# Kernel optimization log

Measured on AMD Instinct MI355X. Metric: run time of the kernel, lower is better.

## Reference

```python
import jax, jax.numpy as jnp
import numpy as np

# cfg constants (init_kwargs)
NMS_THRESH = 0.6
CONF_THRESH = 0.05
TOPN = 1000           # nms_thresh_topN: pre-NMS cap and post-NMS cap
NUM_CLASSES = 80
CLS_OFFSET = 4096.0   # > max image coord; class-aware NMS via coordinate offset


def setup_inputs() -> dict:
    key = jax.random.key(0)
    k0, k1, k2, k3 = jax.random.split(key, 4)
    B, H, W, C = 16, 128, 128, NUM_CLASSES
    N = H * W
    image_h, image_w = 1024, 1024
    # anchor-point pixel coordinates for this FPN level
    locations = jax.random.uniform(k0, (N, 2), dtype=jnp.float32) * 1024.0
    pred_cls = jax.random.normal(k1, (B, H, W, C), dtype=jnp.float32)
    # (l, t, r, b) distances are positive
    pred_boxes = jax.random.uniform(k2, (B, H, W, 4), dtype=jnp.float32) * 64.0
    pred_centerness = jax.random.normal(k3, (B, H, W), dtype=jnp.float32)
    return {"locations": locations, "pred_cls": pred_cls, "pred_boxes": pred_boxes,
            "pred_centerness": pred_centerness, "image_h": image_h, "image_w": image_w}


def _pairwise_iou(b):  # b: [K, 4] xyxy
    x1, y1, x2, y2 = b[:, 0], b[:, 1], b[:, 2], b[:, 3]
    area = jnp.maximum(x2 - x1, 0.0) * jnp.maximum(y2 - y1, 0.0)
    ix1 = jnp.maximum(x1[:, None], x1[None, :])
    iy1 = jnp.maximum(y1[:, None], y1[None, :])
    ix2 = jnp.minimum(x2[:, None], x2[None, :])
    iy2 = jnp.minimum(y2[:, None], y2[None, :])
    inter = jnp.maximum(ix2 - ix1, 0.0) * jnp.maximum(iy2 - iy1, 0.0)
    return inter / (area[:, None] + area[None, :] - inter + 1e-9)


def _nms_keep(iou, valid):
    # greedy NMS over score-descending candidates; iou: [B,K,K], valid: [B,K] bool
    K = iou.shape[-1]
    ar = jnp.arange(K)

    def body(i, keep):
        iou_i = jax.lax.dynamic_index_in_dim(iou, i, axis=1, keepdims=False)  # [B,K]
        keep_i = jnp.take(keep, i, axis=1)                                    # [B]
        sup = (iou_i > NMS_THRESH) & (ar[None, :] > i) & keep_i[:, None]
        return keep & ~sup

    return jax.lax.fori_loop(0, K, body, valid)


def reference(locations, pred_cls, pred_boxes, pred_centerness, image_h, image_w):
    B, H, W, C = pred_cls.shape
    N = H * W
    cls = jax.nn.sigmoid(pred_cls.reshape(B, N, C))
    ctr = jax.nn.sigmoid(pred_centerness.reshape(B, N))
    boxes = pred_boxes.reshape(B, N, 4)
    scores = cls * ctr[:, :, None]                    # [B,N,C]
    mask = cls > CONF_THRESH
    neg = jnp.asarray(-jnp.inf, scores.dtype)
    flat = jnp.where(mask, scores, neg).reshape(B, N * C)
    # pre-NMS top-K over masked (location, class) candidates; emulates
    # cls_mask_top_n = clamp(mask.sum(), max=topN) + topk in the torch code
    vals, idx = jax.lax.top_k(flat, TOPN)             # [B,K]
    valid = jnp.isfinite(vals)
    loc_i = idx // C                                  # location index
    lab = idx % C + 1                                 # 1-based class label
    pb = jnp.take_along_axis(boxes, loc_i[:, :, None], axis=1)   # [B,K,4] (l,t,r,b)
    locs = locations[loc_i]                                       # [B,K,2]
    x1 = jnp.clip(locs[..., 0] - pb[..., 0], 0.0, image_w - 1)
    y1 = jnp.clip(locs[..., 1] - pb[..., 1], 0.0, image_h - 1)
    x2 = jnp.clip(locs[..., 0] + pb[..., 2], 0.0, image_w - 1)
    y2 = jnp.clip(locs[..., 1] + pb[..., 3], 0.0, image_h - 1)
    det = jnp.stack([x1, y1, x2, y2], axis=-1)        # [B,K,4] xyxy, clipped
    score = jnp.where(valid, vals, 0.0)
    # sort by score descending for greedy NMS
    order = jnp.argsort(-score, axis=1)
    score = jnp.take_along_axis(score, order, axis=1)
    valid = jnp.take_along_axis(valid, order, axis=1)
    lab = jnp.take_along_axis(lab, order, axis=1)
    det = jnp.take_along_axis(det, order[:, :, None], axis=1)
    # per-class NMS via class-offset trick (boxes of different classes never overlap)
    iou = jax.vmap(_pairwise_iou)(det + lab.astype(det.dtype)[:, :, None] * CLS_OFFSET)
    keep = _nms_keep(iou, valid) & valid
    # final topN (nms_thresh_topN) is a no-op here: candidates <= TOPN already
    boxes_out = det * keep[:, :, None].astype(det.dtype)
    scores_out = jnp.where(keep, score, 0.0)
    labels_out = jnp.where(keep, lab, 0)
    return boxes_out, scores_out, labels_out
```

## Files before the change

kernel.cpp:

```cpp
#include <hip/hip_runtime.h>

#define B_    16
#define N_    16384
#define C_    80
#define NC_   (N_ * C_)
#define TOPN_ 1000
#define SEGCAP_ 4096
#define T0_   0.70f
#define T0KEY_ 0x3F333333u
#define RKEY_  0x3E800000u
#define NBIN_  4096

#define OFF_CNT    0u
#define ZERO_BYTES 8192u
#define OFF_CAND   8192u
#define OFF_DET    4202496u
#define OFF_DETO   4464640u
#define OFF_SCORE  4726784u
#define OFF_LAB    4792320u
#define OFF_VALID  4857856u
#define OFF_COL    4859904u

__device__ __forceinline__ float sigm(float x) { return 1.0f / (1.0f + expf(-x)); }

__device__ __forceinline__ int binof(unsigned key) {
    int b = (int)((key - RKEY_) >> 12);
    return b > (NBIN_ - 1) ? (NBIN_ - 1) : b;
}
__device__ __forceinline__ unsigned key_lb(int b) {
    return RKEY_ + ((unsigned)b << 12);
}

__global__ __launch_bounds__(256, 4) void k_pass1(const float* __restrict__ cls,
                                                  const float* __restrict__ ctr,
                                                  unsigned* __restrict__ cntp,
                                                  unsigned long long* __restrict__ cand) {
    __shared__ float xh[64];
    __shared__ float sbv[64];
    __shared__ unsigned long long stage[512];
    __shared__ unsigned lcnt, gbase, lcw;
    const int blk = blockIdx.x, t = threadIdx.x;
    const int b = blk >> 8, k = blk & 255;
    const int shard = k & 7;
    if (t == 0) lcnt = 0;
    if (t < 64) {
        float sc = sigm(ctr[b * N_ + k * 64 + t]);
        sbv[t] = sc;
        float q = T0_ / sc;
        xh[t] = (q < 1.f) ? (logf(q / (1.f - q)) - 1e-3f) : 3.0e38f;
    }
    __syncthreads();
    const float4* p = (const float4*)(cls + (size_t)b * NC_ + (size_t)k * 5120);
    float4 v[5];
    #pragma unroll
    for (int i = 0; i < 5; ++i) v[i] = p[5 * t + i];
    const int r = t >> 2;
    const float thr = xh[r];
    float mx = v[0].x;
    #pragma unroll
    for (int i = 0; i < 5; ++i)
        mx = fmaxf(mx, fmaxf(fmaxf(v[i].x, v[i].y), fmaxf(v[i].z, v[i].w)));
    if (mx >= thr) {
        const float sb = sbv[r];
        #pragma unroll
        for (int i = 0; i < 5; ++i) {
            float xs[4] = {v[i].x, v[i].y, v[i].z, v[i].w};
            #pragma unroll
            for (int j = 0; j < 4; ++j) {
                if (xs[j] >= thr) {
                    float sapx = sb * __builtin_amdgcn_rcpf(1.f + __expf(-xs[j]));
                    if (sapx >= T0_ * 0.999f) {
                        float s = sigm(xs[j]);
                        unsigned key = __float_as_uint(s * sb);
                        if (key >= T0KEY_) {
                            unsigned pos = atomicAdd(&lcnt, 1u);
                            if (pos < 512u) {
                                unsigned e = (unsigned)(k * 5120 + (5 * t + i) * 4 + j);
                                stage[pos] = ((unsigned long long)key << 32) |
                                             (unsigned long long)(0xFFFFFFFFu - e);
                            }
                        }
                    }
                }
            }
        }
    }
    __syncthreads();
    if (t == 0) {
        unsigned lc = lcnt; if (lc > 512u) lc = 512u;
        gbase = atomicAdd(&cntp[b * 128 + shard * 16], lc);
        lcw = lc;
    }
    __syncthreads();
    unsigned long long* seg = cand + ((size_t)(b * 8 + shard) << 12);
    for (unsigned i = t; i < lcw; i += 256) {
        unsigned gp = gbase + i;
        if (gp < SEGCAP_) seg[gp] = stage[i];
    }
}

__global__ __launch_bounds__(256) void k_rescue(const float* __restrict__ cls,
                                                const float* __restrict__ ctr,
                                                unsigned* __restrict__ cntp,
                                                unsigned long long* __restrict__ cand) {
    const int blk = blockIdx.x, t = threadIdx.x;
    const int b = blk >> 7, k = blk & 127;
    {
        unsigned tot = 0;
        #pragma unroll
        for (int s = 0; s < 8; ++s) tot += cntp[b * 128 + s * 16];
        if (tot >= (unsigned)TOPN_) return;
    }
    const int shard = k & 7;
    __shared__ float xh[128];
    __shared__ float sbv[128];
    __shared__ unsigned long long stage[1024];
    __shared__ unsigned lcnt, gbase, lcw;
    if (t == 0) lcnt = 0;
    if (t < 128) {
        float sc = sigm(ctr[b * N_ + k * 128 + t]);
        sbv[t] = sc;
        float q = 0.25f / sc;
        xh[t] = (q < 1.f) ? (logf(q / (1.f - q)) - 1e-3f) : 3.0e38f;
    }
    __syncthreads();
    const float4* p = (const float4*)(cls + (size_t)b * NC_ + (size_t)k * 10240);
    for (int f = t; f < 2560; f += 256) {
        float4 v = p[f];
        int nl = f / 20;
        float thr = xh[nl];
        float mx = fmaxf(fmaxf(v.x, v.y), fmaxf(v.z, v.w));
        if (mx >= thr) {
            float sb = sbv[nl];
            float xs[4] = {v.x, v.y, v.z, v.w};
            #pragma unroll
            for (int j = 0; j < 4; ++j) {
                if (xs[j] >= thr) {
                    float s = sigm(xs[j]);
                    if (s > 0.05f) {
                        unsigned key = __float_as_uint(s * sb);
                        if (key >= RKEY_ && key < T0KEY_) {
                            unsigned pos = atomicAdd(&lcnt, 1u);
                            if (pos < 1024u) {
                                unsigned e = (unsigned)(k * 2560 + f) * 4u + (unsigned)j;
                                stage[pos] = ((unsigned long long)key << 32) |
                                             (unsigned long long)(0xFFFFFFFFu - e);
                            }
                        }
                    }
                }
            }
        }
    }
    __syncthreads();
    if (t == 0) {
        unsigned lc = lcnt; if (lc > 1024u) lc = 1024u;
        gbase = atomicAdd(&cntp[b * 128 + shard * 16], lc);
        lcw = lc;
    }
    __syncthreads();
    unsigned long long* seg = cand + ((size_t)(b * 8 + shard) << 12);
    for (unsigned i = t; i < lcw; i += 256) {
        unsigned gp = gbase + i;
        if (gp < SEGCAP_) seg[gp] = stage[i];
    }
}

__global__ __launch_bounds__(1024) void k_select(
        const unsigned long long* __restrict__ cand, const unsigned* __restrict__ cntp,
        const float* __restrict__ boxes, const float* __restrict__ locs,
        const int* __restrict__ ph, const int* __restrict__ pw,
        float4* __restrict__ det, float4* __restrict__ deto,
        float* __restrict__ score, int* __restrict__ lab,
        unsigned long long* __restrict__ validmask) {
    __shared__ unsigned hbin[NBIN_];
    __shared__ unsigned binBase[NBIN_];
    __shared__ unsigned long long srt[2048];
    __shared__ unsigned long long srt2[1024];
    __shared__ unsigned csh[8];
    __shared__ unsigned Lsh;
    const int b = blockIdx.x, t = threadIdx.x;
    if (t < 8) { unsigned cc = cntp[b * 128 + t * 16]; csh[t] = cc > SEGCAP_ ? SEGCAP_ : cc; }
    #pragma unroll
    for (int i = 0; i < 4; ++i) hbin[t + 1024 * i] = 0;
    srt[t] = 0ull; srt[t + 1024] = 0ull;
    srt2[t] = 0ull;
    __syncthreads();
    const unsigned long long* g = cand + ((size_t)b << 15);
    for (int s = 0; s < 8; ++s) {
        unsigned cc = csh[s];
        const unsigned long long* gs = g + ((size_t)s << 12);
        for (unsigned o = t; o < cc; o += 1024)
            atomicAdd(&hbin[binof((unsigned)(gs[o] >> 32))], 1u);
    }
    __syncthreads();
    if (t < 64) {
        const int l = t;
        unsigned cs = 0;
        for (int i = 0; i < 64; ++i) cs += hbin[64 * l + i];
        unsigned S = cs;
        #pragma unroll
        for (int off = 1; off < 64; off <<= 1) {
            unsigned y = __shfl_down(S, off, 64);
            if (l + off < 64) S += y;
        }
        unsigned acc = S - cs;
        int bc_l = NBIN_;
        for (int b2 = 63; b2 >= 0; --b2) {
            int bin = 64 * l + b2;
            binBase[bin] = acc;
            if (acc < (unsigned)TOPN_) bc_l = bin;
            acc += hbin[bin];
        }
        #pragma unroll
        for (int off = 1; off < 64; off <<= 1) {
            int y = __shfl_down(bc_l, off, 64);
            bc_l = bc_l < y ? bc_l : y;
        }
        if (l == 0) Lsh = key_lb(bc_l < NBIN_ ? bc_l : 0);
    }
    __syncthreads();
    const unsigned Lk = Lsh;
    for (int s = 0; s < 8; ++s) {
        unsigned cc = csh[s];
        const unsigned long long* gs = g + ((size_t)s << 12);
        for (unsigned o = t; o < cc; o += 1024) {
            unsigned long long comp = gs[o];
            unsigned key = (unsigned)(comp >> 32);
            if (key >= Lk) {
                unsigned slot = atomicAdd(&binBase[binof(key)], 1u);
                if (slot < 2048u) srt[slot] = comp;
            }
        }
    }
    __syncthreads();
    #pragma unroll
    for (int pp = 0; pp < 2; ++pp) {
        unsigned p = (unsigned)t + 1024u * pp;
        unsigned long long comp = srt[p];
        if (comp) {
            int bin = binof((unsigned)(comp >> 32));
            unsigned endq = binBase[bin];
            unsigned pop = hbin[bin];
            unsigned beg = endq - pop;
            unsigned end2 = endq > 2048u ? 2048u : endq;
            unsigned rank = 0;
            for (unsigned j = beg; j < end2; ++j) rank += (srt[j] > comp);
            unsigned pos = beg + rank;
            if (pos < 1024u) srt2[pos] = comp;
        }
    }
    __syncthreads();
    unsigned long long comp = srt2[t];
    unsigned key = (unsigned)(comp >> 32);
    float4 d = {0.f, 0.f, 0.f, 0.f}, doff = {0.f, 0.f, 0.f, 0.f};
    float sc = 0.f; int lb = 0;
    if (key) {
        unsigned idx = 0xFFFFFFFFu - (unsigned)comp;
        unsigned loc = idx / (unsigned)C_;
        unsigned cc = idx - loc * (unsigned)C_;
        lb = (int)cc + 1;
        float4 pb = ((const float4*)boxes)[(size_t)b * N_ + loc];
        float lx = locs[2 * loc], ly = locs[2 * loc + 1];
        float Wm1 = (float)(pw[0] - 1), Hm1 = (float)(ph[0] - 1);
        d.x = fminf(fmaxf(lx - pb.x, 0.f), Wm1);
        d.y = fminf(fmaxf(ly - pb.y, 0.f), Hm1);
        d.z = fminf(fmaxf(lx + pb.z, 0.f), Wm1);
        d.w = fminf(fmaxf(ly + pb.w, 0.f), Hm1);
        sc = __uint_as_float(key);
        float off = (float)lb * 4096.0f;
        doff.x = d.x + off; doff.y = d.y + off; doff.z = d.z + off; doff.w = d.w + off;
    }
    unsigned long long ball = __ballot(key != 0u);
    if ((t & 63) == 0) validmask[b * 16 + (t >> 6)] = ball;
    det[b * 1024 + t] = d;
    deto[b * 1024 + t] = doff;
    score[b * 1024 + t] = sc;
    lab[b * 1024 + t] = lb;
}

__global__ void k_col(const float4* __restrict__ deto, unsigned long long* __restrict__ colsup) {
    __shared__ float4 bx[1024];
    const int b = blockIdx.y;
    for (int i = threadIdx.x; i < 1024; i += blockDim.x) bx[i] = deto[b * 1024 + i];
    __syncthreads();
    int t = threadIdx.x;
    int i = blockIdx.x * 16 + (t >> 4);
    int w = t & 15;
    int j0 = w * 64;
    unsigned long long m = 0;
    if (i < TOPN_ && j0 < i) {
        float4 A = bx[i];
        float aA = fmaxf(A.z - A.x, 0.f) * fmaxf(A.w - A.y, 0.f);
        int jmax = i - j0; if (jmax > 64) jmax = 64;
        #pragma unroll 4
        for (int jj = 0; jj < jmax; ++jj) {
            float4 Bv = bx[j0 + jj];
            float aB = fmaxf(Bv.z - Bv.x, 0.f) * fmaxf(Bv.w - Bv.y, 0.f);
            float ix1 = fmaxf(A.x, Bv.x), iy1 = fmaxf(A.y, Bv.y);
            float ix2 = fminf(A.z, Bv.z), iy2 = fminf(A.w, Bv.w);
            float inter = fmaxf(ix2 - ix1, 0.f) * fmaxf(iy2 - iy1, 0.f);
            float iou = inter / (aA + aB - inter + 1e-9f);
            if (iou > 0.6f) m |= (1ull << jj);
        }
    }
    colsup[((size_t)b * 1024 + i) * 16 + w] = m;
}

__global__ __launch_bounds__(1024) void k_nmsout(
        const unsigned long long* __restrict__ colsup,
        const unsigned long long* __restrict__ validmask,
        const float4* __restrict__ det, const float* __restrict__ score,
        const int* __restrict__ lab, float* __restrict__ out) {
    __shared__ unsigned long long keepw[16];
    const int b = blockIdx.x, t = threadIdx.x;
    if (t < 64) {
        const int ii = t;
        const unsigned long long* Cb = colsup + (size_t)b * 16384;
        unsigned long long K[16];
        unsigned long long col[16], coln[16];
        #pragma unroll
        for (int w = 0; w < 16; ++w) col[w] = Cb[(size_t)ii * 16 + w];
        unsigned long long vword[16];
        #pragma unroll
        for (int g = 0; g < 16; ++g) vword[g] = validmask[b * 16 + g];
        #pragma unroll
        for (int g = 0; g < 16; ++g) {
            if (g < 15) {
                #pragma unroll
                for (int w = 0; w < 16; ++w)
                    coln[w] = Cb[(size_t)((g + 1) * 64 + ii) * 16 + w];
            }
            unsigned long long supprior = 0;
            #pragma unroll
            for (int w = 0; w < 16; ++w) if (w < g) supprior |= K[w] & col[w];
            bool alive = (((vword[g] >> ii) & 1ull) != 0) && (supprior == 0);
            unsigned long long diag = col[g];
            unsigned long long undec = __ballot(alive);
            unsigned long long kept = 0;
            while (undec) {
                bool meU = ((undec >> ii) & 1ull) != 0;
                bool supK = (kept & diag) != 0;
                bool anyU = (undec & diag) != 0;
                unsigned long long bkm = __ballot(meU && !supK && !anyU);
                unsigned long long brm = __ballot(meU && supK);
                kept |= bkm;
                undec &= ~(bkm | brm);
            }
            K[g] = kept;
            if (ii == 0) keepw[g] = kept;
            #pragma unroll
            for (int w = 0; w < 16; ++w) col[w] = coln[w];
        }
    }
    __syncthreads();
    if (t < TOPN_) {
        bool kp = ((keepw[t >> 6] >> (t & 63)) & 1ull) != 0;
        float4 d = det[b * 1024 + t];
        ((float4*)out)[(size_t)b * TOPN_ + t] = kp ? d : make_float4(0.f, 0.f, 0.f, 0.f);
        out[B_ * TOPN_ * 4 + b * TOPN_ + t] = kp ? score[b * 1024 + t] : 0.f;
        out[B_ * TOPN_ * 5 + b * TOPN_ + t] = kp ? (float)lab[b * 1024 + t] : 0.f;
    }
}

extern "C" void kernel_launch(void* const* d_in, const int* in_sizes, int n_in,
                              void* d_out, int out_size, void* d_ws, size_t ws_size,
                              hipStream_t stream) {
    (void)in_sizes; (void)n_in; (void)out_size; (void)ws_size;
    const float* locations = (const float*)d_in[0];
    const float* pred_cls  = (const float*)d_in[1];
    const float* pred_box  = (const float*)d_in[2];
    const float* pred_ctr  = (const float*)d_in[3];
    const int*   ph        = (const int*)d_in[4];
    const int*   pw        = (const int*)d_in[5];
    float* out = (float*)d_out;

    char* w = (char*)d_ws;
    unsigned* cntp               = (unsigned*)(w + OFF_CNT);
    unsigned long long* cand     = (unsigned long long*)(w + OFF_CAND);
    float4* det                  = (float4*)(w + OFF_DET);
    float4* deto                 = (float4*)(w + OFF_DETO);
    float* score                 = (float*)(w + OFF_SCORE);
    int* lab                     = (int*)(w + OFF_LAB);
    unsigned long long* validmsk = (unsigned long long*)(w + OFF_VALID);
    unsigned long long* colsup   = (unsigned long long*)(w + OFF_COL);

    hipMemsetAsync(w, 0, ZERO_BYTES, stream);

    k_pass1<<<4096, 256, 0, stream>>>(pred_cls, pred_ctr, cntp, cand);
    k_rescue<<<2048, 256, 0, stream>>>(pred_cls, pred_ctr, cntp, cand);
    k_select<<<B_, 1024, 0, stream>>>(cand, cntp, pred_box, locations, ph, pw,
                                      det, deto, score, lab, validmsk);
    k_col<<<dim3(64, B_), 256, 0, stream>>>(deto, colsup);
    k_nmsout<<<B_, 1024, 0, stream>>>(colsup, validmsk, det, score, lab, out);
}
```

Measured before the change: 196.1 us.

## Fuse rescue, select, IoU and NMS into one per-image tail kernel with class buckets

Merges the rescue pass, top-K selection, pairwise IoU mask construction and greedy NMS into a single 1024-thread block per image. The shared memory of the sort phase is reused for the NMS phase through a union. IoU is now computed only between candidates of the same class, bucketed in shared memory, and stored as short suppressor lists rather than a dense bitmask. This removes three kernel launches and the global-memory round trips for det, score, label and the column masks. In exchange, the rare rescue path becomes a serial 16-block scan, and the suppressor list is capped at 14 per box, which could change results if a box has more same-class overlaps than that.

```diff
diff --git a/kernel.cpp b/kernel.cpp
--- a/kernel.cpp
+++ b/kernel.cpp
@@ -14,12 +14,6 @@
 #define OFF_CNT    0u
 #define ZERO_BYTES 8192u
 #define OFF_CAND   8192u
-#define OFF_DET    4202496u
-#define OFF_DETO   4464640u
-#define OFF_SCORE  4726784u
-#define OFF_LAB    4792320u
-#define OFF_VALID  4857856u
-#define OFF_COL    4859904u
 
 __device__ __forceinline__ float sigm(float x) { return 1.0f / (1.0f + expf(-x)); }
 
@@ -99,105 +93,86 @@
     }
 }
 
-__global__ __launch_bounds__(256) void k_rescue(const float* __restrict__ cls,
-                                                const float* __restrict__ ctr,
-                                                unsigned* __restrict__ cntp,
-                                                unsigned long long* __restrict__ cand) {
-    const int blk = blockIdx.x, t = threadIdx.x;
-    const int b = blk >> 7, k = blk & 127;
-    {
-        unsigned tot = 0;
-        #pragma unroll
-        for (int s = 0; s < 8; ++s) tot += cntp[b * 128 + s * 16];
-        if (tot >= (unsigned)TOPN_) return;
-    }
-    const int shard = k & 7;
-    __shared__ float xh[128];
-    __shared__ float sbv[128];
-    __shared__ unsigned long long stage[1024];
-    __shared__ unsigned lcnt, gbase, lcw;
-    if (t == 0) lcnt = 0;
-    if (t < 128) {
-        float sc = sigm(ctr[b * N_ + k * 128 + t]);
-        sbv[t] = sc;
-        float q = 0.25f / sc;
-        xh[t] = (q < 1.f) ? (logf(q / (1.f - q)) - 1e-3f) : 3.0e38f;
-    }
-    __syncthreads();
-    const float4* p = (const float4*)(cls + (size_t)b * NC_ + (size_t)k * 10240);
-    for (int f = t; f < 2560; f += 256) {
-        float4 v = p[f];
-        int nl = f / 20;
-        float thr = xh[nl];
-        float mx = fmaxf(fmaxf(v.x, v.y), fmaxf(v.z, v.w));
-        if (mx >= thr) {
-            float sb = sbv[nl];
+union TailSMem {
+    struct {
+        unsigned hbin[NBIN_];
+        unsigned binBase[NBIN_];
+        unsigned long long srt[2048];
+        unsigned long long srt2[1024];
+    } s;
+    struct {
+        float4 bxo[1024];
+        unsigned short clsList[1024];
+        unsigned clsStart[81];
+        unsigned clsCur[81];
+        unsigned short supIdx[1024 * 14];
+    } c;
+};
+
+__global__ __launch_bounds__(1024) void k_tail(
+        unsigned long long* __restrict__ cand, unsigned* __restrict__ cntp,
+        const float* __restrict__ boxes, const float* __restrict__ locs,
+        const int* __restrict__ ph, const int* __restrict__ pw,
+        const float* __restrict__ cls, const float* __restrict__ ctr,
+        float* __restrict__ out) {
+    __shared__ TailSMem u;
+    __shared__ unsigned csh[8];
+    __shared__ unsigned Lsh;
+    __shared__ unsigned long long keepw[16];
+    const int b = blockIdx.x, t = threadIdx.x;
+
+    if (t < 8) { unsigned cc = cntp[b * 128 + t * 16]; csh[t] = cc > SEGCAP_ ? SEGCAP_ : cc; }
+    __syncthreads();
+    unsigned tot = 0;
+    #pragma unroll
+    for (int s = 0; s < 8; ++s) tot += csh[s];
+    if (tot < (unsigned)TOPN_) {
+        const float4* p = (const float4*)(cls + (size_t)b * NC_);
+        for (unsigned f = t; f < (unsigned)(NC_ / 4); f += 1024) {
+            float4 v = p[f];
+            unsigned nl = f / 20;
+            float sb = sigm(ctr[b * N_ + nl]);
             float xs[4] = {v.x, v.y, v.z, v.w};
             #pragma unroll
             for (int j = 0; j < 4; ++j) {
-                if (xs[j] >= thr) {
-                    float s = sigm(xs[j]);
-                    if (s > 0.05f) {
-                        unsigned key = __float_as_uint(s * sb);
-                        if (key >= RKEY_ && key < T0KEY_) {
-                            unsigned pos = atomicAdd(&lcnt, 1u);
-                            if (pos < 1024u) {
-                                unsigned e = (unsigned)(k * 2560 + f) * 4u + (unsigned)j;
-                                stage[pos] = ((unsigned long long)key << 32) |
-                                             (unsigned long long)(0xFFFFFFFFu - e);
-                            }
+                float s = sigm(xs[j]);
+                if (s > 0.05f) {
+                    unsigned key = __float_as_uint(s * sb);
+                    if (key >= RKEY_ && key < T0KEY_) {
+                        int sh = t & 7;
+                        unsigned pos = atomicAdd(&cntp[b * 128 + sh * 16], 1u);
+                        if (pos < SEGCAP_) {
+                            unsigned e = 4u * f + (unsigned)j;
+                            cand[((size_t)(b * 8 + sh) << 12) + pos] =
+                                ((unsigned long long)key << 32) |
+                                (unsigned long long)(0xFFFFFFFFu - e);
                         }
                     }
                 }
             }
         }
-    }
-    __syncthreads();
-    if (t == 0) {
-        unsigned lc = lcnt; if (lc > 1024u) lc = 1024u;
-        gbase = atomicAdd(&cntp[b * 128 + shard * 16], lc);
-        lcw = lc;
-    }
-    __syncthreads();
-    unsigned long long* seg = cand + ((size_t)(b * 8 + shard) << 12);
-    for (unsigned i = t; i < lcw; i += 256) {
-        unsigned gp = gbase + i;
-        if (gp < SEGCAP_) seg[gp] = stage[i];
-    }
-}
-
-__global__ __launch_bounds__(1024) void k_select(
-        const unsigned long long* __restrict__ cand, const unsigned* __restrict__ cntp,
-        const float* __restrict__ boxes, const float* __restrict__ locs,
-        const int* __restrict__ ph, const int* __restrict__ pw,
-        float4* __restrict__ det, float4* __restrict__ deto,
-        float* __restrict__ score, int* __restrict__ lab,
-        unsigned long long* __restrict__ validmask) {
-    __shared__ unsigned hbin[NBIN_];
-    __shared__ unsigned binBase[NBIN_];
-    __shared__ unsigned long long srt[2048];
-    __shared__ unsigned long long srt2[1024];
-    __shared__ unsigned csh[8];
-    __shared__ unsigned Lsh;
-    const int b = blockIdx.x, t = threadIdx.x;
-    if (t < 8) { unsigned cc = cntp[b * 128 + t * 16]; csh[t] = cc > SEGCAP_ ? SEGCAP_ : cc; }
-    #pragma unroll
-    for (int i = 0; i < 4; ++i) hbin[t + 1024 * i] = 0;
-    srt[t] = 0ull; srt[t + 1024] = 0ull;
-    srt2[t] = 0ull;
+        __syncthreads();
+        if (t < 8) { unsigned cc = cntp[b * 128 + t * 16]; csh[t] = cc > SEGCAP_ ? SEGCAP_ : cc; }
+        __syncthreads();
+    }
+
+    #pragma unroll
+    for (int i = 0; i < 4; ++i) u.s.hbin[t + 1024 * i] = 0;
+    u.s.srt[t] = 0ull; u.s.srt[t + 1024] = 0ull;
+    u.s.srt2[t] = 0ull;
     __syncthreads();
     const unsigned long long* g = cand + ((size_t)b << 15);
     for (int s = 0; s < 8; ++s) {
         unsigned cc = csh[s];
         const unsigned long long* gs = g + ((size_t)s << 12);
         for (unsigned o = t; o < cc; o += 1024)
-            atomicAdd(&hbin[binof((unsigned)(gs[o] >> 32))], 1u);
+            atomicAdd(&u.s.hbin[binof((unsigned)(gs[o] >> 32))], 1u);
     }
     __syncthreads();
     if (t < 64) {
         const int l = t;
         unsigned cs = 0;
-        for (int i = 0; i < 64; ++i) cs += hbin[64 * l + i];
+        for (int i = 0; i < 64; ++i) cs += u.s.hbin[64 * l + i];
         unsigned S = cs;
         #pragma unroll
         for (int off = 1; off < 64; off <<= 1) {
@@ -208,9 +183,9 @@
         int bc_l = NBIN_;
         for (int b2 = 63; b2 >= 0; --b2) {
             int bin = 64 * l + b2;
-            binBase[bin] = acc;
+            u.s.binBase[bin] = acc;
             if (acc < (unsigned)TOPN_) bc_l = bin;
-            acc += hbin[bin];
+            acc += u.s.hbin[bin];
         }
         #pragma unroll
         for (int off = 1; off < 64; off <<= 1) {
@@ -228,8 +203,8 @@
             unsigned long long comp = gs[o];
             unsigned key = (unsigned)(comp >> 32);
             if (key >= Lk) {
-                unsigned slot = atomicAdd(&binBase[binof(key)], 1u);
-                if (slot < 2048u) srt[slot] = comp;
+                unsigned slot = atomicAdd(&u.s.binBase[binof(key)], 1u);
+                if (slot < 2048u) u.s.srt[slot] = comp;
             }
         }
     }
@@ -237,29 +212,29 @@
     #pragma unroll
     for (int pp = 0; pp < 2; ++pp) {
         unsigned p = (unsigned)t + 1024u * pp;
-        unsigned long long comp = srt[p];
+        unsigned long long comp = u.s.srt[p];
         if (comp) {
             int bin = binof((unsigned)(comp >> 32));
-            unsigned endq = binBase[bin];
-            unsigned pop = hbin[bin];
+            unsigned endq = u.s.binBase[bin];
+            unsigned pop = u.s.hbin[bin];
             unsigned beg = endq - pop;
             unsigned end2 = endq > 2048u ? 2048u : endq;
             unsigned rank = 0;
-            for (unsigned j = beg; j < end2; ++j) rank += (srt[j] > comp);
+            for (unsigned j = beg; j < end2; ++j) rank += (u.s.srt[j] > comp);
             unsigned pos = beg + rank;
-            if (pos < 1024u) srt2[pos] = comp;
-        }
-    }
-    __syncthreads();
-    unsigned long long comp = srt2[t];
+            if (pos < 1024u) u.s.srt2[pos] = comp;
+        }
+    }
+    __syncthreads();
+    unsigned long long comp = u.s.srt2[t];
     unsigned key = (unsigned)(comp >> 32);
     float4 d = {0.f, 0.f, 0.f, 0.f}, doff = {0.f, 0.f, 0.f, 0.f};
     float sc = 0.f; int lb = 0;
     if (key) {
         unsigned idx = 0xFFFFFFFFu - (unsigned)comp;
         unsigned loc = idx / (unsigned)C_;
-        unsigned cc = idx - loc * (unsigned)C_;
-        lb = (int)cc + 1;
+        unsigned cc2 = idx - loc * (unsigned)C_;
+        lb = (int)cc2 + 1;
         float4 pb = ((const float4*)boxes)[(size_t)b * N_ + loc];
         float lx = locs[2 * loc], ly = locs[2 * loc + 1];
         float Wm1 = (float)(pw[0] - 1), Hm1 = (float)(ph[0] - 1);
@@ -271,71 +246,67 @@
         float off = (float)lb * 4096.0f;
         doff.x = d.x + off; doff.y = d.y + off; doff.z = d.z + off; doff.w = d.w + off;
     }
-    unsigned long long ball = __ballot(key != 0u);
-    if ((t & 63) == 0) validmask[b * 16 + (t >> 6)] = ball;
-    det[b * 1024 + t] = d;
-    deto[b * 1024 + t] = doff;
-    score[b * 1024 + t] = sc;
-    lab[b * 1024 + t] = lb;
-}
-
-__global__ void k_col(const float4* __restrict__ deto, unsigned long long* __restrict__ colsup) {
-    __shared__ float4 bx[1024];
-    const int b = blockIdx.y;
-    for (int i = threadIdx.x; i < 1024; i += blockDim.x) bx[i] = deto[b * 1024 + i];
-    __syncthreads();
-    int t = threadIdx.x;
-    int i = blockIdx.x * 16 + (t >> 4);
-    int w = t & 15;
-    int j0 = w * 64;
-    unsigned long long m = 0;
-    if (i < TOPN_ && j0 < i) {
-        float4 A = bx[i];
+    const bool valid = (key != 0u);
+    __syncthreads();
+
+    u.c.bxo[t] = doff;
+    if (t < 81) { u.c.clsStart[t] = 0; }
+    __syncthreads();
+    if (lb > 0) atomicAdd(&u.c.clsStart[lb], 1u);
+    __syncthreads();
+    if (t == 0) {
+        unsigned run = 0;
+        for (int c2 = 1; c2 <= 80; ++c2) {
+            unsigned v = u.c.clsStart[c2];
+            u.c.clsStart[c2] = run; u.c.clsCur[c2] = run;
+            run += v;
+        }
+    }
+    __syncthreads();
+    if (lb > 0) {
+        unsigned pos = atomicAdd(&u.c.clsCur[lb], 1u);
+        u.c.clsList[pos] = (unsigned short)t;
+    }
+    __syncthreads();
+    unsigned nsup = 0;
+    if (valid) {
+        float4 A = doff;
         float aA = fmaxf(A.z - A.x, 0.f) * fmaxf(A.w - A.y, 0.f);
-        int jmax = i - j0; if (jmax > 64) jmax = 64;
-        #pragma unroll 4
-        for (int jj = 0; jj < jmax; ++jj) {
-            float4 Bv = bx[j0 + jj];
-            float aB = fmaxf(Bv.z - Bv.x, 0.f) * fmaxf(Bv.w - Bv.y, 0.f);
-            float ix1 = fmaxf(A.x, Bv.x), iy1 = fmaxf(A.y, Bv.y);
-            float ix2 = fminf(A.z, Bv.z), iy2 = fminf(A.w, Bv.w);
-            float inter = fmaxf(ix2 - ix1, 0.f) * fmaxf(iy2 - iy1, 0.f);
-            float iou = inter / (aA + aB - inter + 1e-9f);
-            if (iou > 0.6f) m |= (1ull << jj);
-        }
-    }
-    colsup[((size_t)b * 1024 + i) * 16 + w] = m;
-}
-
-__global__ __launch_bounds__(1024) void k_nmsout(
-        const unsigned long long* __restrict__ colsup,
-        const unsigned long long* __restrict__ validmask,
-        const float4* __restrict__ det, const float* __restrict__ score,
-        const int* __restrict__ lab, float* __restrict__ out) {
-    __shared__ unsigned long long keepw[16];
-    const int b = blockIdx.x, t = threadIdx.x;
-    if (t < 64) {
-        const int ii = t;
-        const unsigned long long* Cb = colsup + (size_t)b * 16384;
-        unsigned long long K[16];
-        unsigned long long col[16], coln[16];
-        #pragma unroll
-        for (int w = 0; w < 16; ++w) col[w] = Cb[(size_t)ii * 16 + w];
-        unsigned long long vword[16];
-        #pragma unroll
-        for (int g = 0; g < 16; ++g) vword[g] = validmask[b * 16 + g];
-        #pragma unroll
-        for (int g = 0; g < 16; ++g) {
-            if (g < 15) {
-                #pragma unroll
-                for (int w = 0; w < 16; ++w)
-                    coln[w] = Cb[(size_t)((g + 1) * 64 + ii) * 16 + w];
-            }
-            unsigned long long supprior = 0;
-            #pragma unroll
-            for (int w = 0; w < 16; ++w) if (w < g) supprior |= K[w] & col[w];
-            bool alive = (((vword[g] >> ii) & 1ull) != 0) && (supprior == 0);
-            unsigned long long diag = col[g];
+        unsigned beg = u.c.clsStart[lb], end = u.c.clsCur[lb];
+        for (unsigned q = beg; q < end; ++q) {
+            int j = (int)u.c.clsList[q];
+            if (j < t) {
+                float4 Bv = u.c.bxo[j];
+                float aB = fmaxf(Bv.z - Bv.x, 0.f) * fmaxf(Bv.w - Bv.y, 0.f);
+                float ix1 = fmaxf(A.x, Bv.x), iy1 = fmaxf(A.y, Bv.y);
+                float ix2 = fminf(A.z, Bv.z), iy2 = fminf(A.w, Bv.w);
+                float inter = fmaxf(ix2 - ix1, 0.f) * fmaxf(iy2 - iy1, 0.f);
+                float iou = inter / (aA + aB - inter + 1e-9f);
+                if (iou > 0.6f) {
+                    if (nsup < 14u) u.c.supIdx[t * 14 + nsup] = (unsigned short)j;
+                    ++nsup;
+                }
+            }
+        }
+        if (nsup > 14u) nsup = 14u;
+    }
+    __syncthreads();
+
+    const int gof = t >> 6, ii = t & 63;
+    for (int gg = 0; gg < 16; ++gg) {
+        if (gof == gg) {
+            const unsigned base = (unsigned)(gg << 6);
+            unsigned long long diag = 0;
+            bool supP = false;
+            for (unsigned q = 0; q < nsup; ++q) {
+                unsigned j = (unsigned)u.c.supIdx[t * 14 + q];
+                if (j < base) {
+                    if ((keepw[j >> 6] >> (j & 63)) & 1ull) supP = true;
+                } else {
+                    diag |= 1ull << (j & 63);
+                }
+            }
+            bool alive = valid && !supP;
             unsigned long long undec = __ballot(alive);
             unsigned long long kept = 0;
             while (undec) {
@@ -347,19 +318,16 @@
                 kept |= bkm;
                 undec &= ~(bkm | brm);
             }
-            K[g] = kept;
-            if (ii == 0) keepw[g] = kept;
-            #pragma unroll
-            for (int w = 0; w < 16; ++w) col[w] = coln[w];
-        }
-    }
-    __syncthreads();
+            if (ii == 0) keepw[gg] = kept;
+        }
+        __syncthreads();
+    }
+
     if (t < TOPN_) {
-        bool kp = ((keepw[t >> 6] >> (t & 63)) & 1ull) != 0;
-        float4 d = det[b * 1024 + t];
+        bool kp = ((keepw[gof] >> ii) & 1ull) != 0;
         ((float4*)out)[(size_t)b * TOPN_ + t] = kp ? d : make_float4(0.f, 0.f, 0.f, 0.f);
-        out[B_ * TOPN_ * 4 + b * TOPN_ + t] = kp ? score[b * 1024 + t] : 0.f;
-        out[B_ * TOPN_ * 5 + b * TOPN_ + t] = kp ? (float)lab[b * 1024 + t] : 0.f;
+        out[B_ * TOPN_ * 4 + b * TOPN_ + t] = kp ? sc : 0.f;
+        out[B_ * TOPN_ * 5 + b * TOPN_ + t] = kp ? (float)lb : 0.f;
     }
 }
 
@@ -376,21 +344,12 @@
     float* out = (float*)d_out;
 
     char* w = (char*)d_ws;
-    unsigned* cntp               = (unsigned*)(w + OFF_CNT);
-    unsigned long long* cand     = (unsigned long long*)(w + OFF_CAND);
-    float4* det                  = (float4*)(w + OFF_DET);
-    float4* deto                 = (float4*)(w + OFF_DETO);
-    float* score                 = (float*)(w + OFF_SCORE);
-    int* lab                     = (int*)(w + OFF_LAB);
-    unsigned long long* validmsk = (unsigned long long*)(w + OFF_VALID);
-    unsigned long long* colsup   = (unsigned long long*)(w + OFF_COL);
+    unsigned* cntp           = (unsigned*)(w + OFF_CNT);
+    unsigned long long* cand = (unsigned long long*)(w + OFF_CAND);
 
     hipMemsetAsync(w, 0, ZERO_BYTES, stream);
 
     k_pass1<<<4096, 256, 0, stream>>>(pred_cls, pred_ctr, cntp, cand);
-    k_rescue<<<2048, 256, 0, stream>>>(pred_cls, pred_ctr, cntp, cand);
-    k_select<<<B_, 1024, 0, stream>>>(cand, cntp, pred_box, locations, ph, pw,
-                                      det, deto, score, lab, validmsk);
-    k_col<<<dim3(64, B_), 256, 0, stream>>>(deto, colsup);
-    k_nmsout<<<B_, 1024, 0, stream>>>(colsup, validmsk, det, score, lab, out);
-}
+    k_tail<<<B_, 1024, 0, stream>>>(cand, cntp, pred_box, locations, ph, pw,
+                                    pred_cls, pred_ctr, out);
+}
```

After: 166.2 us. 15.3% less time.
